# Performance work log

Measured on AMD Instinct MI355X. Metric: run time of the kernel, lower is better.

Reference implementation:

```python
import jax, jax.numpy as jnp
import numpy as np

D = 1024   # 'heads' arg = d_model
H = 4      # no_of_heads
DH = D // H
B, T = 4, 2048


def _ln(x, g, b, eps=1e-5):
    m = x.mean(-1, keepdims=True)
    v = ((x - m) ** 2).mean(-1, keepdims=True)
    return (x - m) / jnp.sqrt(v + eps) * g + b


def _heads_proj(x, W):
    # x: [B,T,D]; W: [H,dh,dh] per-head nn.Linear weights (out = x @ W^T)
    b, t, c = x.shape
    h, dh, _ = W.shape
    xh = x.reshape(b, t, h, dh)  # channel slices i*dh:(i+1)*dh == reshape
    return jnp.einsum('bthd,hed->bthe', xh, W)


def _self_attn(x, wq, wk, wv, masked):
    q = _heads_proj(x, wq)
    k = _heads_proj(x, wk)
    v = _heads_proj(x, wv)
    dh = wq.shape[-1]
    s = jnp.einsum('bthe,bshe->bhts', q, k) * dh ** -0.5  # [B,H,T,T]
    if masked:
        t = x.shape[1]
        causal = jnp.tril(jnp.ones((t, t), dtype=bool))
        s = jnp.where(causal, s, -jnp.inf)
    a = jax.nn.softmax(s, axis=-1)
    o = jnp.einsum('bhts,bshd->bthd', a, v)
    return o.reshape(x.shape)


def _cross_attn(ctx, x, wq, wk, wv):
    # NOTE: the original CrossAttention applies NO softmax — faithful copy.
    q = _heads_proj(x, wq)
    k = _heads_proj(ctx, wk)
    v = _heads_proj(ctx, wv)
    dh = wq.shape[-1]
    s = jnp.einsum('bthe,bshe->bhts', q, k) * dh ** -0.5
    o = jnp.einsum('bhts,bshd->bthd', s, v)
    return o.reshape(x.shape)


def _ffn(x, w1, b1, w2, b2):
    return jax.nn.relu(x @ w1.T + b1) @ w2.T + b2


def setup_inputs() -> dict:
    key = jax.random.key(0)
    ks = jax.random.split(key, 16)
    sc = 0.02
    d = {
        'context': jax.random.normal(ks[0], (B, T, D), jnp.float32),
        'X': jax.random.normal(ks[1], (B, T, D), jnp.float32),
        'dec_wq': jax.random.normal(ks[2], (H, DH, DH), jnp.float32) * sc,
        'dec_wk': jax.random.normal(ks[3], (H, DH, DH), jnp.float32) * sc,
        'dec_wv': jax.random.normal(ks[4], (H, DH, DH), jnp.float32) * sc,
        'x_wq': jax.random.normal(ks[5], (H, DH, DH), jnp.float32) * sc,
        'x_wk': jax.random.normal(ks[6], (H, DH, DH), jnp.float32) * sc,
        'x_wv': jax.random.normal(ks[7], (H, DH, DH), jnp.float32) * sc,
        'enc_wq': jax.random.normal(ks[8], (H, DH, DH), jnp.float32) * sc,
        'enc_wk': jax.random.normal(ks[9], (H, DH, DH), jnp.float32) * sc,
        'enc_wv': jax.random.normal(ks[10], (H, DH, DH), jnp.float32) * sc,
        'dec_w1': jax.random.normal(ks[11], (4 * D, D), jnp.float32) * sc,
        'dec_b1': jnp.zeros((4 * D,), jnp.float32),
        'dec_w2': jax.random.normal(ks[12], (D, 4 * D), jnp.float32) * sc,
        'dec_b2': jnp.zeros((D,), jnp.float32),
        'enc_w1': jax.random.normal(ks[13], (4 * D, D), jnp.float32) * sc,
        'enc_b1': jnp.zeros((4 * D,), jnp.float32),
        'enc_w2': jax.random.normal(ks[14], (D, 4 * D), jnp.float32) * sc,
        'enc_b2': jnp.zeros((D,), jnp.float32),
        'dec_ln1_g': jnp.ones((D,), jnp.float32), 'dec_ln1_b': jnp.zeros((D,), jnp.float32),
        'dec_ln2_g': jnp.ones((D,), jnp.float32), 'dec_ln2_b': jnp.zeros((D,), jnp.float32),
        'dec_ln3_g': jnp.ones((D,), jnp.float32), 'dec_ln3_b': jnp.zeros((D,), jnp.float32),
        'enc_ln1_g': jnp.ones((D,), jnp.float32), 'enc_ln1_b': jnp.zeros((D,), jnp.float32),
        'enc_ln2_g': jnp.ones((D,), jnp.float32), 'enc_ln2_b': jnp.zeros((D,), jnp.float32),
    }
    return d


def reference(context, X, dec_wq, dec_wk, dec_wv, x_wq, x_wk, x_wv,
              enc_wq, enc_wk, enc_wv, dec_w1, dec_b1, dec_w2, dec_b2,
              enc_w1, enc_b1, enc_w2, enc_b2,
              dec_ln1_g, dec_ln1_b, dec_ln2_g, dec_ln2_b, dec_ln3_g, dec_ln3_b,
              enc_ln1_g, enc_ln1_b, enc_ln2_g, enc_ln2_b):
    # Dropout (p=0.1) treated as identity (eval mode).
    x1 = _ln(X + _self_attn(X, dec_wq, dec_wk, dec_wv, True), dec_ln1_g, dec_ln1_b)
    # EncoderBlock on context (non-masked self-attn + FFN)
    c = _ln(context + _self_attn(context, enc_wq, enc_wk, enc_wv, False), enc_ln1_g, enc_ln1_b)
    c = _ln(c + _ffn(c, enc_w1, enc_b1, enc_w2, enc_b2), enc_ln2_g, enc_ln2_b)
    x2 = _ln(x1 + _cross_attn(c, x1, x_wq, x_wk, x_wv), dec_ln2_g, dec_ln2_b)
    out = _ln(x2 + _ffn(x2, dec_w1, dec_b1, dec_w2, dec_b2), dec_ln3_g, dec_ln3_b)
    return (c, out)
```

## Files before the change

kernel.cpp:

```cpp
#include <hip/hip_runtime.h>
#include <hip/hip_bf16.h>

typedef unsigned short u16;
typedef __bf16 bf16x8 __attribute__((ext_vector_type(8)));
typedef unsigned short u16x8 __attribute__((ext_vector_type(8)));
typedef unsigned short u16x4 __attribute__((ext_vector_type(4)));
typedef float f32x4 __attribute__((ext_vector_type(4)));

#define DI static __device__ __forceinline__

DI u16 f2bf(float f) {
    unsigned u = __builtin_bit_cast(unsigned, f);
    u += 0x7FFFu + ((u >> 16) & 1u);
    return (u16)(u >> 16);
}
DI float bf2f(u16 u) {
    unsigned x = ((unsigned)u) << 16;
    return __builtin_bit_cast(float, x);
}
DI u16x8 ld8_f32(const float* __restrict__ p) {
    const float4 a = *(const float4*)p;
    const float4 b = *(const float4*)(p + 4);
    u16x8 r = { f2bf(a.x), f2bf(a.y), f2bf(a.z), f2bf(a.w),
                f2bf(b.x), f2bf(b.y), f2bf(b.z), f2bf(b.w) };
    return r;
}
DI f32x4 mfma16(u16x8 a, u16x8 b, f32x4 c) {
    return __builtin_amdgcn_mfma_f32_16x16x32_bf16(
        __builtin_bit_cast(bf16x8, a), __builtin_bit_cast(bf16x8, b), c, 0, 0, 0);
}

__global__ void __launch_bounds__(256) k_cast(const float* __restrict__ in,
                                              u16* __restrict__ out, long n4) {
    long i = (long)blockIdx.x * 256 + threadIdx.x;
    if (i >= n4) return;
    const float4 v = *(const float4*)(in + i * 4);
    u16x4 o = { f2bf(v.x), f2bf(v.y), f2bf(v.z), f2bf(v.w) };
    *(u16x4*)(out + i * 4) = o;
}

template <int AF32, int BF32>
__global__ void __launch_bounds__(256, 2) k_gemm_bt(
    const void* __restrict__ Ap, long lda,
    const void* __restrict__ Bp, long ldb,
    float* __restrict__ Cf, u16* __restrict__ Cb, long ldc,
    const float* __restrict__ bias, int relu, int accum, float alpha, int K,
    int Hdiv, long sAb, long sAh, long sBb, long sBh, long sCb, long sCh)
{
    __shared__ __align__(16) u16 As[128 * 72];
    __shared__ __align__(16) u16 Bs[128 * 72];
    const int tid  = threadIdx.x;
    const int lane = tid & 63, wave = tid >> 6;
    const int r16  = lane & 15, quad = lane >> 4;
    const int wr   = (wave >> 1) * 64, wc = (wave & 1) * 64;
    const int zb = blockIdx.z / Hdiv, zh = blockIdx.z % Hdiv;
    const long aoff = (long)zb * sAb + (long)zh * sAh + (long)blockIdx.x * 128 * lda;
    const long boff = (long)zb * sBb + (long)zh * sBh + (long)blockIdx.y * 128 * ldb;
    const u16*   A16 = (const u16*)Ap + aoff;
    const float* A32 = (const float*)Ap + aoff;
    const u16*   B16 = (const u16*)Bp + boff;
    const float* B32 = (const float*)Bp + boff;
    const long coff = (long)zb * sCb + (long)zh * sCh +
                      (long)blockIdx.x * 128 * ldc + (long)blockIdx.y * 128;

    f32x4 acc[4][4];
#pragma unroll
    for (int i = 0; i < 4; i++)
#pragma unroll
        for (int j = 0; j < 4; j++) acc[i][j] = f32x4{0.f, 0.f, 0.f, 0.f};

    const int st_row = tid >> 3;
    const int st_col = (tid & 7) * 8;

    u16x8 ar0, ar1, ar2, ar3, br0, br1, br2, br3;

#define LDAB(KS)                                                              \
    do {                                                                      \
        const long kk0_ = (long)(KS) * 64 + st_col;                           \
        if constexpr (AF32) {                                                 \
            ar0 = ld8_f32(A32 + (long)(st_row)      * lda + kk0_);            \
            ar1 = ld8_f32(A32 + (long)(st_row + 32) * lda + kk0_);            \
            ar2 = ld8_f32(A32 + (long)(st_row + 64) * lda + kk0_);            \
            ar3 = ld8_f32(A32 + (long)(st_row + 96) * lda + kk0_);            \
        } else {                                                              \
            ar0 = *(const u16x8*)(A16 + (long)(st_row)      * lda + kk0_);    \
            ar1 = *(const u16x8*)(A16 + (long)(st_row + 32) * lda + kk0_);    \
            ar2 = *(const u16x8*)(A16 + (long)(st_row + 64) * lda + kk0_);    \
            ar3 = *(const u16x8*)(A16 + (long)(st_row + 96) * lda + kk0_);    \
        }                                                                     \
        if constexpr (BF32) {                                                 \
            br0 = ld8_f32(B32 + (long)(st_row)      * ldb + kk0_);            \
            br1 = ld8_f32(B32 + (long)(st_row + 32) * ldb + kk0_);            \
            br2 = ld8_f32(B32 + (long)(st_row + 64) * ldb + kk0_);            \
            br3 = ld8_f32(B32 + (long)(st_row + 96) * ldb + kk0_);            \
        } else {                                                              \
            br0 = *(const u16x8*)(B16 + (long)(st_row)      * ldb + kk0_);    \
            br1 = *(const u16x8*)(B16 + (long)(st_row + 32) * ldb + kk0_);    \
            br2 = *(const u16x8*)(B16 + (long)(st_row + 64) * ldb + kk0_);    \
            br3 = *(const u16x8*)(B16 + (long)(st_row + 96) * ldb + kk0_);    \
        }                                                                     \
    } while (0)

#define STAB()                                                                \
    do {                                                                      \
        u16* ap_ = As + st_row * 72 + st_col;                                 \
        *(u16x8*)(ap_)            = ar0;                                      \
        *(u16x8*)(ap_ + 32 * 72)  = ar1;                                      \
        *(u16x8*)(ap_ + 64 * 72)  = ar2;                                      \
        *(u16x8*)(ap_ + 96 * 72)  = ar3;                                      \
        u16* bp_ = Bs + st_row * 72 + st_col;                                 \
        *(u16x8*)(bp_)            = br0;                                      \
        *(u16x8*)(bp_ + 32 * 72)  = br1;                                      \
        *(u16x8*)(bp_ + 64 * 72)  = br2;                                      \
        *(u16x8*)(bp_ + 96 * 72)  = br3;                                      \
    } while (0)

    LDAB(0);
    STAB();
    __syncthreads();

    const int nks = K >> 6;
    for (int ks = 0; ks < nks; ks++) {
        const bool more = (ks + 1 < nks);
        if (more) LDAB(ks + 1);
#pragma unroll
        for (int kk = 0; kk < 64; kk += 32) {
            u16x8 af[4], bfr[4];
#pragma unroll
            for (int i = 0; i < 4; i++)
                af[i] = *(const u16x8*)(As + (wr + i * 16 + r16) * 72 + kk + 8 * quad);
#pragma unroll
            for (int j = 0; j < 4; j++)
                bfr[j] = *(const u16x8*)(Bs + (wc + j * 16 + r16) * 72 + kk + 8 * quad);
#pragma unroll
            for (int i = 0; i < 4; i++)
#pragma unroll
                for (int j = 0; j < 4; j++)
                    acc[i][j] = mfma16(af[i], bfr[j], acc[i][j]);
        }
        __syncthreads();
        if (more) {
            STAB();
            __syncthreads();
        }
    }
#undef LDAB
#undef STAB

#pragma unroll
    for (int i = 0; i < 4; i++) {
#pragma unroll
        for (int j = 0; j < 4; j++) {
            const int gcol = wc + j * 16 + r16;
            const float bv = bias ? bias[blockIdx.y * 128 + gcol] : 0.f;
#pragma unroll
            for (int r = 0; r < 4; r++) {
                const long o = coff + (long)(wr + i * 16 + quad * 4 + r) * ldc + gcol;
                float v = acc[i][j][r] * alpha + bv;
                if (accum) v += Cf[o];
                if (relu) v = fmaxf(v, 0.f);
                if (Cf) Cf[o] = v;
                if (Cb) Cb[o] = f2bf(v);
            }
        }
    }
}

template <int NSEG>
__global__ void __launch_bounds__(256) k_proj(
    const float* __restrict__ A,
    const float* __restrict__ W0, const float* __restrict__ W1,
    const float* __restrict__ W2,
    u16* __restrict__ C0, u16* __restrict__ C1, u16* __restrict__ C2)
{
    __shared__ __align__(16) u16 As[128 * 72];
    __shared__ __align__(16) u16 Bs[128 * 72];
    const int tid  = threadIdx.x;
    const int lane = tid & 63, wave = tid >> 6;
    const int r16  = lane & 15, quad = lane >> 4;
    const int wr   = (wave >> 1) * 64, wc = (wave & 1) * 64;
    const int seg = blockIdx.y >> 1, yy = blockIdx.y & 1, h = blockIdx.z;
    const float* W = (NSEG >= 3 && seg == 2) ? W2 : (seg == 1 ? W1 : W0);
    u16*         C = (NSEG >= 3 && seg == 2) ? C2 : (seg == 1 ? C1 : C0);
    const float* Ab = A + (long)blockIdx.x * 128 * 1024 + h * 256;
    const float* Bb = W + (long)h * 65536 + yy * 128 * 256;
    u16* Cp = C + (long)blockIdx.x * 128 * 1024 + h * 256 + yy * 128;

    f32x4 acc[4][4];
#pragma unroll
    for (int i = 0; i < 4; i++)
#pragma unroll
        for (int j = 0; j < 4; j++) acc[i][j] = f32x4{0.f, 0.f, 0.f, 0.f};

    const int st_row = tid >> 3, st_col = (tid & 7) * 8;

    for (int k0 = 0; k0 < 256; k0 += 64) {
#pragma unroll
        for (int r = 0; r < 4; r++) {
            const int row = st_row + 32 * r;
            *(u16x8*)(As + row * 72 + st_col) = ld8_f32(Ab + (long)row * 1024 + k0 + st_col);
            *(u16x8*)(Bs + row * 72 + st_col) = ld8_f32(Bb + (long)row * 256 + k0 + st_col);
        }
        __syncthreads();
#pragma unroll
        for (int kk = 0; kk < 64; kk += 32) {
            u16x8 af[4], bfr[4];
#pragma unroll
            for (int i = 0; i < 4; i++)
                af[i] = *(const u16x8*)(As + (wr + i * 16 + r16) * 72 + kk + 8 * quad);
#pragma unroll
            for (int j = 0; j < 4; j++)
                bfr[j] = *(const u16x8*)(Bs + (wc + j * 16 + r16) * 72 + kk + 8 * quad);
#pragma unroll
            for (int i = 0; i < 4; i++)
#pragma unroll
                for (int j = 0; j < 4; j++)
                    acc[i][j] = mfma16(af[i], bfr[j], acc[i][j]);
        }
        __syncthreads();
    }

#pragma unroll
    for (int i = 0; i < 4; i++)
#pragma unroll
        for (int j = 0; j < 4; j++)
#pragma unroll
            for (int r = 0; r < 4; r++)
                Cp[(long)(wr + i * 16 + quad * 4 + r) * 1024 + wc + j * 16 + r16] =
                    f2bf(acc[i][j][r]);
}

template <int MASKED>
__global__ void __launch_bounds__(256, 2) k_attn(
    const u16* __restrict__ Q, const u16* __restrict__ Kg, const u16* __restrict__ Vt,
    u16* __restrict__ O, int T, float scale)
{
    const int D = 1024;
    __shared__ __align__(16) u16 Ks[64 * 264];
    __shared__ __align__(16) u16 VsT[256 * 72];
    __shared__ __align__(16) u16 Ps[4][16 * 72];
    const int tid = threadIdx.x, lane = tid & 63, wave = tid >> 6;
    const int r16 = lane & 15, quad = lane >> 4;

    const int fid = blockIdx.x + (blockIdx.y << 5) + (blockIdx.z << 7);
    const int swz = ((fid & 7) << 6) | (fid >> 3);
    const int bx = swz & 31, hh = (swz >> 5) & 3, bb = swz >> 7;

    const long base   = ((long)bb * T) * D + hh * 256;
    const long vtbase = ((long)(bb * 4 + hh) * 256) * 2048;
    const int qr0 = bx * 64 + wave * 16;

    u16x8 qf[8];
#pragma unroll
    for (int ks = 0; ks < 8; ks++)
        qf[ks] = *(const u16x8*)(Q + base + (long)(qr0 + r16) * D + ks * 32 + 8 * quad);

    f32x4 oacc[16];
#pragma unroll
    for (int nt = 0; nt < 16; nt++) oacc[nt] = f32x4{0.f, 0.f, 0.f, 0.f};
    f32x4 lacc = f32x4{0.f, 0.f, 0.f, 0.f};
    const u16x8 ones8 = {0x3F80, 0x3F80, 0x3F80, 0x3F80,
                         0x3F80, 0x3F80, 0x3F80, 0x3F80};

    const int krow = tid >> 5, kcol = (tid & 31) * 8;
    const int vrow = tid >> 3, vcol = (tid & 7) * 8;
    const int nkb = MASKED ? (bx + 1) : (T / 64);

    const u16* kg = Kg + base;
    const u16* vg = Vt + vtbase + (long)vrow * 2048 + vcol;

    uint4 kr0, kr1, kr2, kr3, kr4, kr5, kr6, kr7;
    uint4 vr0, vr1, vr2, vr3, vr4, vr5, vr6, vr7;

#define LD_KV(KB)                                                          \
    do {                                                                   \
        const u16* kp_ = kg + ((long)(KB) * 64 + krow) * D + kcol;         \
        kr0 = *(const uint4*)(kp_);                                        \
        kr1 = *(const uint4*)(kp_ + 8 * D);                                \
        kr2 = *(const uint4*)(kp_ + 16 * D);                               \
        kr3 = *(const uint4*)(kp_ + 24 * D);                               \
        kr4 = *(const uint4*)(kp_ + 32 * D);                               \
        kr5 = *(const uint4*)(kp_ + 40 * D);                               \
        kr6 = *(const uint4*)(kp_ + 48 * D);                               \
        kr7 = *(const uint4*)(kp_ + 56 * D);                               \
        const u16* vp_ = vg + (KB) * 64;                                   \
        vr0 = *(const uint4*)(vp_);                                        \
        vr1 = *(const uint4*)(vp_ + 32 * 2048);                            \
        vr2 = *(const uint4*)(vp_ + 64 * 2048);                            \
        vr3 = *(const uint4*)(vp_ + 96 * 2048);                            \
        vr4 = *(const uint4*)(vp_ + 128 * 2048);                           \
        vr5 = *(const uint4*)(vp_ + 160 * 2048);                           \
        vr6 = *(const uint4*)(vp_ + 192 * 2048);                           \
        vr7 = *(const uint4*)(vp_ + 224 * 2048);                           \
    } while (0)

#define ST_KV()                                                            \
    do {                                                                   \
        u16* kq_ = Ks + krow * 264 + kcol;                                 \
        *(uint4*)(kq_)            = kr0;                                   \
        *(uint4*)(kq_ + 8 * 264)  = kr1;                                   \
        *(uint4*)(kq_ + 16 * 264) = kr2;                                   \
        *(uint4*)(kq_ + 24 * 264) = kr3;                                   \
        *(uint4*)(kq_ + 32 * 264) = kr4;                                   \
        *(uint4*)(kq_ + 40 * 264) = kr5;                                   \
        *(uint4*)(kq_ + 48 * 264) = kr6;                                   \
        *(uint4*)(kq_ + 56 * 264) = kr7;                                   \
        u16* vq_ = VsT + vrow * 72 + vcol;                                 \
        *(uint4*)(vq_)            = vr0;                                   \
        *(uint4*)(vq_ + 32 * 72)  = vr1;                                   \
        *(uint4*)(vq_ + 64 * 72)  = vr2;                                   \
        *(uint4*)(vq_ + 96 * 72)  = vr3;                                   \
        *(uint4*)(vq_ + 128 * 72) = vr4;                                   \
        *(uint4*)(vq_ + 160 * 72) = vr5;                                   \
        *(uint4*)(vq_ + 192 * 72) = vr6;                                   \
        *(uint4*)(vq_ + 224 * 72) = vr7;                                   \
    } while (0)

    LD_KV(0);
    ST_KV();
    __syncthreads();

    u16* const pw = &Ps[wave][0];

    for (int kb = 0; kb < nkb; kb++) {
        const bool more = (kb + 1 < nkb);
        if (more) LD_KV(kb + 1);

        f32x4 s0 = f32x4{0.f,0.f,0.f,0.f}, s1 = f32x4{0.f,0.f,0.f,0.f};
        f32x4 s2 = f32x4{0.f,0.f,0.f,0.f}, s3 = f32x4{0.f,0.f,0.f,0.f};
#pragma unroll
        for (int ks = 0; ks < 8; ks++) {
            const u16x8 a = qf[ks];
            const u16* kp = Ks + r16 * 264 + ks * 32 + 8 * quad;
            s0 = mfma16(a, *(const u16x8*)(kp),            s0);
            s1 = mfma16(a, *(const u16x8*)(kp + 16 * 264), s1);
            s2 = mfma16(a, *(const u16x8*)(kp + 32 * 264), s2);
            s3 = mfma16(a, *(const u16x8*)(kp + 48 * 264), s3);
        }

        const bool domask = MASKED && (kb == nkb - 1);

#pragma unroll
        for (int r = 0; r < 4; r++) {
            float a0 = s0[r] * scale, a1 = s1[r] * scale;
            float a2 = s2[r] * scale, a3 = s3[r] * scale;
            if (domask) {
                const int qi = qr0 + quad * 4 + r;
                const int kb0 = kb * 64;
                if (kb0 + r16 > qi)      a0 = -1e30f;
                if (kb0 + 16 + r16 > qi) a1 = -1e30f;
                if (kb0 + 32 + r16 > qi) a2 = -1e30f;
                if (kb0 + 48 + r16 > qi) a3 = -1e30f;
            }
            const float p0 = __expf(fminf(a0, 30.f));
            const float p1 = __expf(fminf(a1, 30.f));
            const float p2 = __expf(fminf(a2, 30.f));
            const float p3 = __expf(fminf(a3, 30.f));
            u16* pr = pw + (quad * 4 + r) * 72 + r16;
            pr[0]  = f2bf(p0);
            pr[16] = f2bf(p1);
            pr[32] = f2bf(p2);
            pr[48] = f2bf(p3);
        }

        const u16* pp = pw + r16 * 72 + 8 * quad;
        const u16x8 pfA = *(const u16x8*)(pp);
        const u16x8 pfB = *(const u16x8*)(pp + 32);
        lacc = mfma16(pfA, ones8, lacc);
        lacc = mfma16(pfB, ones8, lacc);
#pragma unroll
        for (int nt = 0; nt < 16; nt++) {
            const u16* vp = VsT + (nt * 16 + r16) * 72 + 8 * quad;
            oacc[nt] = mfma16(pfA, *(const u16x8*)(vp),      oacc[nt]);
            oacc[nt] = mfma16(pfB, *(const u16x8*)(vp + 32), oacc[nt]);
        }

        __syncthreads();
        if (more) {
            ST_KV();
            __syncthreads();
        }
    }
#undef LD_KV
#undef ST_KV

#pragma unroll
    for (int r = 0; r < 4; r++) lacc[r] = 1.f / lacc[r];
#pragma unroll
    for (int nt = 0; nt < 16; nt++)
#pragma unroll
        for (int r = 0; r < 4; r++)
            O[base + (long)(qr0 + quad * 4 + r) * D + nt * 16 + r16] =
                f2bf(oacc[nt][r] * lacc[r]);
}

template <int XF32, int RF32>
__global__ void __launch_bounds__(256) k_addln(
    const void* __restrict__ Xp, const void* __restrict__ Rp,
    const float* __restrict__ G, const float* __restrict__ Bv,
    float* __restrict__ Yf, u16* __restrict__ Yb)
{
    const int tid = threadIdx.x;
    const long off = (long)blockIdx.x * 1024 + tid * 4;
    float v[4];
    if constexpr (XF32) {
        const float4 a = *(const float4*)((const float*)Xp + off);
        v[0] = a.x; v[1] = a.y; v[2] = a.z; v[3] = a.w;
    } else {
        const u16x4 a = *(const u16x4*)((const u16*)Xp + off);
        v[0] = bf2f(a[0]); v[1] = bf2f(a[1]); v[2] = bf2f(a[2]); v[3] = bf2f(a[3]);
    }
    if constexpr (RF32) {
        const float4 b = *(const float4*)((const float*)Rp + off);
        v[0] += b.x; v[1] += b.y; v[2] += b.z; v[3] += b.w;
    } else {
        const u16x4 b = *(const u16x4*)((const u16*)Rp + off);
        v[0] += bf2f(b[0]); v[1] += bf2f(b[1]); v[2] += bf2f(b[2]); v[3] += bf2f(b[3]);
    }
    float s1 = v[0] + v[1] + v[2] + v[3];
    float s2 = v[0]*v[0] + v[1]*v[1] + v[2]*v[2] + v[3]*v[3];
#pragma unroll
    for (int m = 1; m < 64; m <<= 1) { s1 += __shfl_xor(s1, m); s2 += __shfl_xor(s2, m); }
    __shared__ float red[8];
    if ((tid & 63) == 0) { red[(tid >> 6) * 2] = s1; red[(tid >> 6) * 2 + 1] = s2; }
    __syncthreads();
    s1 = red[0] + red[2] + red[4] + red[6];
    s2 = red[1] + red[3] + red[5] + red[7];
    const float mean = s1 * (1.f / 1024.f);
    const float rstd = rsqrtf(s2 * (1.f / 1024.f) - mean * mean + 1e-5f);
    const float4 g  = *(const float4*)(G + tid * 4);
    const float4 be = *(const float4*)(Bv + tid * 4);
    const float o0 = (v[0] - mean) * rstd * g.x + be.x;
    const float o1 = (v[1] - mean) * rstd * g.y + be.y;
    const float o2 = (v[2] - mean) * rstd * g.z + be.z;
    const float o3 = (v[3] - mean) * rstd * g.w + be.w;
    if (Yf) { float4 of = {o0, o1, o2, o3}; *(float4*)(Yf + off) = of; }
    if (Yb) { u16x4 ob = {f2bf(o0), f2bf(o1), f2bf(o2), f2bf(o3)}; *(u16x4*)(Yb + off) = ob; }
}

__global__ void __launch_bounds__(256) k_transpose(const u16* __restrict__ Xin,
                                                   u16* __restrict__ Y)
{
    __shared__ u16 tile[32][33];
    const int tx = threadIdx.x & 31, ty = threadIdx.x >> 5;
    const int t0 = blockIdx.x * 32, e0 = blockIdx.y * 32, bh = blockIdx.z;
    const int b = bh >> 2, h = bh & 3;
#pragma unroll
    for (int i = 0; i < 4; i++)
        tile[ty + 8 * i][tx] =
            Xin[((long)(b * 2048 + t0 + ty + 8 * i)) * 1024 + h * 256 + e0 + tx];
    __syncthreads();
#pragma unroll
    for (int i = 0; i < 4; i++)
        Y[((long)bh * 256 + e0 + ty + 8 * i) * 2048 + t0 + tx] = tile[tx][ty + 8 * i];
}

#define GEMM(AF, BF, Aptr, lda, Bptr, ldb, pCf, pCb, ldc, bias, relu, accum, alpha, \
             M, N, K, Z, Hdiv, sAb, sAh, sBb, sBh, sCb, sCh)                        \
    k_gemm_bt<AF, BF><<<dim3((M) / 128, (N) / 128, (Z)), dim3(256), 0, stream>>>(   \
        (const void*)(Aptr), (lda), (const void*)(Bptr), (ldb), (pCf), (pCb),       \
        (ldc), (bias), (relu), (accum), (alpha), (K), (Hdiv),                       \
        (long)(sAb), (long)(sAh), (long)(sBb), (long)(sBh), (long)(sCb), (long)(sCh))

extern "C" void kernel_launch(void* const* d_in, const int* in_sizes, int n_in,
                              void* d_out, int out_size, void* d_ws, size_t ws_size,
                              hipStream_t stream)
{
    const int Bn = 4, T = 2048, D = 1024, H = 4, DH = 256;
    const long BTD = (long)Bn * T * D;
    const long MB = 1024 * 1024;

    const float* ctx = (const float*)d_in[0];
    const float* X   = (const float*)d_in[1];
    const float* Wh[9]; for (int i = 0; i < 9; i++) Wh[i] = (const float*)d_in[2 + i];
    const float* dec_w1 = (const float*)d_in[11]; const float* dec_b1 = (const float*)d_in[12];
    const float* dec_w2 = (const float*)d_in[13]; const float* dec_b2 = (const float*)d_in[14];
    const float* enc_w1 = (const float*)d_in[15]; const float* enc_b1 = (const float*)d_in[16];
    const float* enc_w2 = (const float*)d_in[17]; const float* enc_b2 = (const float*)d_in[18];
    const float* ln[10]; for (int i = 0; i < 10; i++) ln[i] = (const float*)d_in[19 + i];
    (void)in_sizes; (void)n_in; (void)out_size; (void)ws_size;

    float* outC = (float*)d_out;
    float* outY = (float*)d_out + BTD;

    char* w = (char*)d_ws;
    u16*   qb   = (u16*)(w);
    u16*   kb   = (u16*)(w + 16 * MB);
    u16*   vb   = (u16*)(w + 32 * MB);
    u16*   tmpB = (u16*)(w + 48 * MB);
    float* fout = (float*)(w);
    u16*   w1b  = (u16*)(w + 16 * MB);
    u16*   w2b  = (u16*)(w + 24 * MB);
    u16*   hb   = (u16*)(w + 32 * MB);
    u16*   Kt2  = (u16*)(w + 32 * MB);
    u16*   crossO= (u16*)(w + 32 * MB);
    u16*   Vt2  = (u16*)(w + 48 * MB);
    u16*   Nm   = (u16*)(w + 64 * MB);
    u16*   x1b  = (u16*)(w + 66 * MB);
    u16*   t2b  = (u16*)(w + 82 * MB);

    k_proj<3><<<dim3(64, 6, 4), dim3(256), 0, stream>>>(
        X, Wh[0], Wh[1], Wh[2], qb, kb, vb);
    k_transpose<<<dim3(T / 32, DH / 32, Bn * H), dim3(256), 0, stream>>>(vb, tmpB);
    k_attn<1><<<dim3(T / 64, H, Bn), dim3(256), 0, stream>>>(qb, kb, tmpB, vb, T, 0.0625f);
    k_addln<1, 0><<<dim3(Bn * T), dim3(256), 0, stream>>>(X, vb, ln[0], ln[1], nullptr, x1b);

    k_proj<3><<<dim3(64, 6, 4), dim3(256), 0, stream>>>(
        ctx, Wh[6], Wh[7], Wh[8], qb, kb, vb);
    k_transpose<<<dim3(T / 32, DH / 32, Bn * H), dim3(256), 0, stream>>>(vb, tmpB);
    k_attn<0><<<dim3(T / 64, H, Bn), dim3(256), 0, stream>>>(qb, kb, tmpB, vb, T, 0.0625f);
    k_addln<1, 0><<<dim3(Bn * T), dim3(256), 0, stream>>>(ctx, vb, ln[6], ln[7], nullptr, t2b);

    k_cast<<<dim3(4096), dim3(256), 0, stream>>>(enc_w1, w1b, 1048576);
    k_cast<<<dim3(4096), dim3(256), 0, stream>>>(enc_w2, w2b, 1048576);
    for (int c = 0; c < 2; c++) {
        const long moff = (long)c * 4096 * 1024;
        GEMM(0, 0, t2b + moff, D, w1b, D, nullptr, hb, 4096, enc_b1, 1, 0, 1.f,
             4096, 4096, 1024, 1, 1, 0, 0, 0, 0, 0, 0);
        GEMM(0, 0, hb, 4096, w2b, 4096, fout, nullptr, 1024, enc_b2, 0, 0, 1.f,
             4096, 1024, 4096, 1, 1, 0, 0, 0, 0, 0, 0);
        k_addln<0, 1><<<dim3(4096), dim3(256), 0, stream>>>(
            t2b + moff, fout, ln[8], ln[9], outC + moff, nullptr);
    }

    GEMM(0, 1, x1b, D, Wh[3], DH, nullptr, qb, D, nullptr, 0, 0, 1.f,
         Bn * T, DH, DH, H, H, 0, DH, 0, DH * DH, 0, DH);
    k_proj<2><<<dim3(64, 4, 4), dim3(256), 0, stream>>>(
        outC, Wh[4], Wh[5], nullptr, kb, t2b, nullptr);
    k_transpose<<<dim3(T / 32, DH / 32, Bn * H), dim3(256), 0, stream>>>(kb, Kt2);
    k_transpose<<<dim3(T / 32, DH / 32, Bn * H), dim3(256), 0, stream>>>(t2b, Vt2);
    GEMM(0, 0, Vt2, T, Kt2, T, nullptr, Nm, DH, nullptr, 0, 0, 1.f,
         DH, DH, T, Bn * H, Bn * H, 0, (long)DH * T, 0, (long)DH * T, 0, DH * DH);
    GEMM(0, 0, qb, D, Nm, DH, nullptr, crossO, D, nullptr, 0, 0, 0.0625f,
         T, DH, DH, Bn * H, H, (long)T * D, DH, (long)H * DH * DH, DH * DH,
         (long)T * D, DH);
    k_addln<0, 0><<<dim3(Bn * T), dim3(256), 0, stream>>>(x1b, crossO, ln[2], ln[3], nullptr, t2b);

    k_cast<<<dim3(4096), dim3(256), 0, stream>>>(dec_w1, w1b, 1048576);
    k_cast<<<dim3(4096), dim3(256), 0, stream>>>(dec_w2, w2b, 1048576);
    for (int c = 0; c < 2; c++) {
        const long moff = (long)c * 4096 * 1024;
        GEMM(0, 0, t2b + moff, D, w1b, D, nullptr, hb, 4096, dec_b1, 1, 0, 1.f,
             4096, 4096, 1024, 1, 1, 0, 0, 0, 0, 0, 0);
        GEMM(0, 0, hb, 4096, w2b, 4096, fout, nullptr, 1024, dec_b2, 0, 0, 1.f,
             4096, 1024, 4096, 1, 1, 0, 0, 0, 0, 0, 0);
        k_addln<0, 1><<<dim3(4096), dim3(256), 0, stream>>>(
            t2b + moff, fout, ln[4], ln[5], outY + moff, nullptr);
    }
}
```

Measured before the change: 963.0 us.

## Use 128-query-row attention blocks with 8 waves sharing K/V tiles

The attention kernel now runs 512 threads (8 waves) per block and covers 128 query rows, so each K/V tile staged in shared memory serves twice as many queries. This halves global K/V traffic per query and halves the per-thread load/store work. The grid becomes a 1D launch of 256 blocks with a reworked swizzle. The causal mask now applies to every block where the tile overlaps a wave's rows, and MFMA sections are wrapped with s_setprio hints. The costs are fewer blocks, which lowers parallelism and occupancy, and more wasted work on masked diagonal tiles.

```diff
diff --git a/kernel.cpp b/kernel.cpp
--- a/kernel.cpp
+++ b/kernel.cpp
@@ -231,24 +231,24 @@
 }
 
 template <int MASKED>
-__global__ void __launch_bounds__(256, 2) k_attn(
+__global__ void __launch_bounds__(512, 2) k_attn(
     const u16* __restrict__ Q, const u16* __restrict__ Kg, const u16* __restrict__ Vt,
     u16* __restrict__ O, int T, float scale)
 {
     const int D = 1024;
     __shared__ __align__(16) u16 Ks[64 * 264];
     __shared__ __align__(16) u16 VsT[256 * 72];
-    __shared__ __align__(16) u16 Ps[4][16 * 72];
+    __shared__ __align__(16) u16 Ps[8][16 * 72];
     const int tid = threadIdx.x, lane = tid & 63, wave = tid >> 6;
     const int r16 = lane & 15, quad = lane >> 4;
 
-    const int fid = blockIdx.x + (blockIdx.y << 5) + (blockIdx.z << 7);
-    const int swz = ((fid & 7) << 6) | (fid >> 3);
-    const int bx = swz & 31, hh = (swz >> 5) & 3, bb = swz >> 7;
+    const int fid = blockIdx.x;
+    const int swz = ((fid & 7) << 5) | (fid >> 3);
+    const int bx = swz & 15, hh = (swz >> 4) & 3, bb = swz >> 6;
 
     const long base   = ((long)bb * T) * D + hh * 256;
     const long vtbase = ((long)(bb * 4 + hh) * 256) * 2048;
-    const int qr0 = bx * 64 + wave * 16;
+    const int qr0 = bx * 128 + wave * 16;
 
     u16x8 qf[8];
 #pragma unroll
@@ -264,56 +264,39 @@
 
     const int krow = tid >> 5, kcol = (tid & 31) * 8;
     const int vrow = tid >> 3, vcol = (tid & 7) * 8;
-    const int nkb = MASKED ? (bx + 1) : (T / 64);
+    const int nkb = MASKED ? (2 * bx + 2) : (T / 64);
 
     const u16* kg = Kg + base;
     const u16* vg = Vt + vtbase + (long)vrow * 2048 + vcol;
 
-    uint4 kr0, kr1, kr2, kr3, kr4, kr5, kr6, kr7;
-    uint4 vr0, vr1, vr2, vr3, vr4, vr5, vr6, vr7;
+    uint4 kr0, kr1, kr2, kr3, vr0, vr1, vr2, vr3;
 
 #define LD_KV(KB)                                                          \
     do {                                                                   \
         const u16* kp_ = kg + ((long)(KB) * 64 + krow) * D + kcol;         \
         kr0 = *(const uint4*)(kp_);                                        \
-        kr1 = *(const uint4*)(kp_ + 8 * D);                                \
-        kr2 = *(const uint4*)(kp_ + 16 * D);                               \
-        kr3 = *(const uint4*)(kp_ + 24 * D);                               \
-        kr4 = *(const uint4*)(kp_ + 32 * D);                               \
-        kr5 = *(const uint4*)(kp_ + 40 * D);                               \
-        kr6 = *(const uint4*)(kp_ + 48 * D);                               \
-        kr7 = *(const uint4*)(kp_ + 56 * D);                               \
+        kr1 = *(const uint4*)(kp_ + 16 * D);                               \
+        kr2 = *(const uint4*)(kp_ + 32 * D);                               \
+        kr3 = *(const uint4*)(kp_ + 48 * D);                               \
         const u16* vp_ = vg + (KB) * 64;                                   \
         vr0 = *(const uint4*)(vp_);                                        \
-        vr1 = *(const uint4*)(vp_ + 32 * 2048);                            \
-        vr2 = *(const uint4*)(vp_ + 64 * 2048);                            \
-        vr3 = *(const uint4*)(vp_ + 96 * 2048);                            \
-        vr4 = *(const uint4*)(vp_ + 128 * 2048);                           \
-        vr5 = *(const uint4*)(vp_ + 160 * 2048);                           \
-        vr6 = *(const uint4*)(vp_ + 192 * 2048);                           \
-        vr7 = *(const uint4*)(vp_ + 224 * 2048);                           \
+        vr1 = *(const uint4*)(vp_ + 64 * 2048);                            \
+        vr2 = *(const uint4*)(vp_ + 128 * 2048);                           \
+        vr3 = *(const uint4*)(vp_ + 192 * 2048);                           \
     } while (0)
 
 #define ST_KV()                                                            \
     do {                                                                   \
         u16* kq_ = Ks + krow * 264 + kcol;                                 \
         *(uint4*)(kq_)            = kr0;                                   \
-        *(uint4*)(kq_ + 8 * 264)  = kr1;                                   \
-        *(uint4*)(kq_ + 16 * 264) = kr2;                                   \
-        *(uint4*)(kq_ + 24 * 264) = kr3;                                   \
-        *(uint4*)(kq_ + 32 * 264) = kr4;                                   \
-        *(uint4*)(kq_ + 40 * 264) = kr5;                                   \
-        *(uint4*)(kq_ + 48 * 264) = kr6;                                   \
-        *(uint4*)(kq_ + 56 * 264) = kr7;                                   \
+        *(uint4*)(kq_ + 16 * 264) = kr1;                                   \
+        *(uint4*)(kq_ + 32 * 264) = kr2;                                   \
+        *(uint4*)(kq_ + 48 * 264) = kr3;                                   \
         u16* vq_ = VsT + vrow * 72 + vcol;                                 \
         *(uint4*)(vq_)            = vr0;                                   \
-        *(uint4*)(vq_ + 32 * 72)  = vr1;                                   \
-        *(uint4*)(vq_ + 64 * 72)  = vr2;                                   \
-        *(uint4*)(vq_ + 96 * 72)  = vr3;                                   \
-        *(uint4*)(vq_ + 128 * 72) = vr4;                                   \
-        *(uint4*)(vq_ + 160 * 72) = vr5;                                   \
-        *(uint4*)(vq_ + 192 * 72) = vr6;                                   \
-        *(uint4*)(vq_ + 224 * 72) = vr7;                                   \
+        *(uint4*)(vq_ + 64 * 72)  = vr1;                                   \
+        *(uint4*)(vq_ + 128 * 72) = vr2;                                   \
+        *(uint4*)(vq_ + 192 * 72) = vr3;                                   \
     } while (0)
 
     LD_KV(0);
@@ -328,6 +311,7 @@
 
         f32x4 s0 = f32x4{0.f,0.f,0.f,0.f}, s1 = f32x4{0.f,0.f,0.f,0.f};
         f32x4 s2 = f32x4{0.f,0.f,0.f,0.f}, s3 = f32x4{0.f,0.f,0.f,0.f};
+        __builtin_amdgcn_s_setprio(1);
 #pragma unroll
         for (int ks = 0; ks < 8; ks++) {
             const u16x8 a = qf[ks];
@@ -337,8 +321,9 @@
             s2 = mfma16(a, *(const u16x8*)(kp + 32 * 264), s2);
             s3 = mfma16(a, *(const u16x8*)(kp + 48 * 264), s3);
         }
-
-        const bool domask = MASKED && (kb == nkb - 1);
+        __builtin_amdgcn_s_setprio(0);
+
+        const bool domask = MASKED && (kb * 64 + 63 > qr0);
 
 #pragma unroll
         for (int r = 0; r < 4; r++) {
@@ -366,6 +351,7 @@
         const u16* pp = pw + r16 * 72 + 8 * quad;
         const u16x8 pfA = *(const u16x8*)(pp);
         const u16x8 pfB = *(const u16x8*)(pp + 32);
+        __builtin_amdgcn_s_setprio(1);
         lacc = mfma16(pfA, ones8, lacc);
         lacc = mfma16(pfB, ones8, lacc);
 #pragma unroll
@@ -374,6 +360,7 @@
             oacc[nt] = mfma16(pfA, *(const u16x8*)(vp),      oacc[nt]);
             oacc[nt] = mfma16(pfB, *(const u16x8*)(vp + 32), oacc[nt]);
         }
+        __builtin_amdgcn_s_setprio(0);
 
         __syncthreads();
         if (more) {
@@ -502,13 +489,13 @@
     k_proj<3><<<dim3(64, 6, 4), dim3(256), 0, stream>>>(
         X, Wh[0], Wh[1], Wh[2], qb, kb, vb);
     k_transpose<<<dim3(T / 32, DH / 32, Bn * H), dim3(256), 0, stream>>>(vb, tmpB);
-    k_attn<1><<<dim3(T / 64, H, Bn), dim3(256), 0, stream>>>(qb, kb, tmpB, vb, T, 0.0625f);
+    k_attn<1><<<dim3(256), dim3(512), 0, stream>>>(qb, kb, tmpB, vb, T, 0.0625f);
     k_addln<1, 0><<<dim3(Bn * T), dim3(256), 0, stream>>>(X, vb, ln[0], ln[1], nullptr, x1b);
 
     k_proj<3><<<dim3(64, 6, 4), dim3(256), 0, stream>>>(
         ctx, Wh[6], Wh[7], Wh[8], qb, kb, vb);
     k_transpose<<<dim3(T / 32, DH / 32, Bn * H), dim3(256), 0, stream>>>(vb, tmpB);
-    k_attn<0><<<dim3(T / 64, H, Bn), dim3(256), 0, stream>>>(qb, kb, tmpB, vb, T, 0.0625f);
+    k_attn<0><<<dim3(256), dim3(512), 0, stream>>>(qb, kb, tmpB, vb, T, 0.0625f);
     k_addln<1, 0><<<dim3(Bn * T), dim3(256), 0, stream>>>(ctx, vb, ln[6], ln[7], nullptr, t2b);
 
     k_cast<<<dim3(4096), dim3(256), 0, stream>>>(enc_w1, w1b, 1048576);
```

Result: no change. 944.3 us (-1.9%).
